# Kernel tuning notes

Hardware: AMD Instinct MI355X
Metric: run time of the kernel (lower is better)

Reference implementation:

```python
import jax, jax.numpy as jnp
import numpy as np

N, D, H, E, K = 4096, 512, 2048, 8, 2  # tokens, input/output dim, expert hidden, num_experts, top_k


def setup_inputs() -> dict:
    key = jax.random.key(0)
    k_x, k_r, k_w1, k_b1, k_w2, k_b2 = jax.random.split(key, 6)
    input_batch = jax.random.normal(k_x, (N, D), dtype=jnp.float32)
    # Router-style top-k selection: guarantees the K expert ids per token are distinct
    # (required by the torch nonzero-based dispatch) and probabilities are a softmax
    # over the selected logits, matching a standard MoE sampler.
    router_logits = jax.random.normal(k_r, (N, E), dtype=jnp.float32)
    top_vals, top_idx = jax.lax.top_k(router_logits, K)
    probabilities = jax.nn.softmax(top_vals, axis=-1)            # [N, K]
    indices = top_idx.astype(jnp.int64)                          # [N, K]
    scale = 0.02
    W1 = scale * jax.random.normal(k_w1, (E, D, H), dtype=jnp.float32)
    b1 = jnp.zeros((E, H), dtype=jnp.float32)
    W2 = scale * jax.random.normal(k_w2, (E, H, D), dtype=jnp.float32)
    b2 = jnp.zeros((E, D), dtype=jnp.float32)
    return {"input_batch": input_batch, "probabilities": probabilities, "indices": indices,
            "W1": W1, "b1": b1, "W2": W2, "b2": b2}


def reference(input_batch, probabilities, indices, W1, b1, W2, b2):
    # Each expert is a dense 2-layer GELU MLP. The torch module gathers the tokens
    # assigned to each expert, runs the expert, concatenates, sorts back to original
    # flattened [N*K] order, applies probability weighting AFTER the experts, then
    # reshapes to [N, K, D] and sums over K. That is mathematically:
    #   out[t] = sum_k probabilities[t, k] * expert_{indices[t, k]}(input_batch[t])
    h = jax.nn.gelu(jnp.einsum('nd,edh->enh', input_batch, W1) + b1[:, None, :])  # [E, N, H]
    y = jnp.einsum('enh,ehd->end', h, W2) + b2[:, None, :]                         # [E, N, D]
    y = jnp.transpose(y, (1, 0, 2))                                                # [N, E, D]
    sel = jnp.take_along_axis(y, indices[:, :, None], axis=1)                      # [N, K, D]
    output = jnp.sum(sel * probabilities[:, :, None], axis=1)                      # [N, D]
    total_loss = jnp.float32(0.0)  # no sampler / expert aux losses in this config
    return output, total_loss
```

## Files before the change

kernel.cpp:

```cpp
#include <hip/hip_runtime.h>
#include <cstdint>
#include <cstddef>

#define NTOK 4096
#define DIMD 512
#define HIDH 2048
#define NEXP 8
#define TOPK 2
#define NSLOT (NTOK*TOPK)
#define SLACK 256
#define YROWS (NSLOT+SLACK)

#define BK2 64

typedef short bf16x8_t __attribute__((ext_vector_type(8)));
typedef float f32x4_t  __attribute__((ext_vector_type(4)));

__device__ __forceinline__ unsigned short f2b(float f){
  unsigned int x = __float_as_uint(f);
  unsigned int r = (x + 0x7FFFu + ((x >> 16) & 1u)) >> 16;
  return (unsigned short)r;
}

__device__ __forceinline__ float gelu_tanh(float x) {
  float z2 = 1.5957691216057308f * fmaf(0.044715f * x, x * x, x);
  return x / (1.f + __expf(-z2));
}

__device__ __forceinline__ void gl_lds16(const void* g, void* l){
  __builtin_amdgcn_global_load_lds((const __attribute__((address_space(1))) void*)g,
                                   (__attribute__((address_space(3))) void*)l, 16, 0, 0);
}


__global__ __launch_bounds__(256) void cvt_x(const float* __restrict__ x, unsigned short* __restrict__ xb){
  int i = blockIdx.x*256 + threadIdx.x;
  if (i >= (NTOK*DIMD)/4) return;
  float4 v = ((const float4*)x)[i];
  ushort4 o; o.x=f2b(v.x); o.y=f2b(v.y); o.z=f2b(v.z); o.w=f2b(v.w);
  ((ushort4*)xb)[i] = o;
}

__global__ __launch_bounds__(256) void transpose_cvt(const float* __restrict__ src,
                                                     unsigned short* __restrict__ dst,
                                                     int R, int C){
  int e = blockIdx.z;
  src += (size_t)e*R*C; dst += (size_t)e*R*C;
  int c0 = blockIdx.x*64, r0 = blockIdx.y*64;
  __shared__ float t[64][65];
  int tr = threadIdx.x >> 4, tc = threadIdx.x & 15;
  #pragma unroll
  for (int i=0;i<4;i++){
    int r = tr + i*16;
    float4 v = *(const float4*)(src + (size_t)(r0 + r)*C + c0 + tc*4);
    t[r][tc*4+0]=v.x; t[r][tc*4+1]=v.y; t[r][tc*4+2]=v.z; t[r][tc*4+3]=v.w;
  }
  __syncthreads();
  #pragma unroll
  for (int i=0;i<4;i++){
    int c = tr + i*16;
    ushort4 o;
    o.x = f2b(t[tc*4+0][c]); o.y = f2b(t[tc*4+1][c]);
    o.z = f2b(t[tc*4+2][c]); o.w = f2b(t[tc*4+3][c]);
    *(ushort4*)(dst + (size_t)(c0 + c)*R + r0 + tc*4) = o;
  }
}


__global__ void count_k(const int* __restrict__ I, int* __restrict__ meta){
  int i = blockIdx.x*256+threadIdx.x;
  if (i < NSLOT) atomicAdd(&meta[I[i]], 1);
}
__global__ void scan_k(int* __restrict__ meta){
  if (threadIdx.x==0 && blockIdx.x==0){
    int s=0;
    for(int e=0;e<NEXP;e++){ meta[16+e]=s; s+=meta[e]; }
  }
}
__global__ void fill_k(const int* __restrict__ I, int* __restrict__ meta,
                       int* __restrict__ tokOf, int* __restrict__ rowOf){
  int i = blockIdx.x*256+threadIdx.x;
  if (i < NSLOT){
    int e = I[i];
    int pos = meta[16+e] + atomicAdd(&meta[8+e], 1);
    tokOf[pos] = i >> 1;
    rowOf[i] = pos;
  }
}



__global__ __launch_bounds__(256,2) void gemm1(
    const unsigned short* __restrict__ Xb, const unsigned short* __restrict__ W1t,
    const float* __restrict__ B1, const int* __restrict__ meta,
    const int* __restrict__ tokOf, unsigned short* __restrict__ H)
{
  const int e = blockIdx.z;
  const int cnt = meta[e];
  const int row0 = blockIdx.y * 128;
  if (row0 >= cnt) return;
  const int off = meta[16+e];
  const int h0 = blockIdx.x * 128;

  extern __shared__ unsigned short sm[];

  const int tid = threadIdx.x;
  const int tr  = tid >> 3;
  const int csw = ((tid & 7) ^ (tr & 7)) << 3;

  const unsigned short* sA[4];
  const unsigned short* sB[4];
  #pragma unroll
  for (int i=0;i<4;i++){
    int slot = min(off + row0 + i*32 + tr, NSLOT-1);
    sA[i] = Xb  + (size_t)tokOf[slot]*DIMD + csw;
    sB[i] = W1t + ((size_t)e*HIDH + h0 + i*32 + tr)*DIMD + csw;
  }

  const int lane = tid & 63, wid = tid >> 6;
  const int wr = (wid >> 1) * 64, wc = (wid & 1) * 64;
  const int l15 = lane & 15, kg = lane >> 4;
  int rowA[4], rowB[4];
  #pragma unroll
  for (int m=0;m<4;m++) rowA[m] = (wr + m*16 + l15) * BK2;
  #pragma unroll
  for (int n=0;n<4;n++) rowB[n] = (wc + n*16 + l15) * BK2;
  const int ch0 = ((kg    ) ^ (l15 & 7)) << 3;
  const int ch1 = ((kg + 4) ^ (l15 & 7)) << 3;

  f32x4_t acc[4][4];
  #pragma unroll
  for (int i=0;i<4;i++){
    #pragma unroll
    for (int j=0;j<4;j++) acc[i][j] = (f32x4_t){0.f,0.f,0.f,0.f};
  }

  auto stage = [&](int buf, int kt){
    unsigned short* d = sm + buf*16384 + tid*8;
    const int k0 = kt * BK2;
    #pragma unroll
    for (int i=0;i<4;i++){
      gl_lds16(sA[i] + k0, d + i*2048);
      gl_lds16(sB[i] + k0, d + 8192 + i*2048);
    }
  };

  auto compute = [&](int buf){
    const unsigned short* SA = sm + buf*16384;
    const unsigned short* SB = SA + 8192;
    #pragma unroll
    for (int h=0; h<2; ++h){
      const int ch = h ? ch1 : ch0;
      bf16x8_t bfr[4], af[4];
      #pragma unroll
      for (int n=0;n<4;n++) bfr[n] = *(const bf16x8_t*)&SB[rowB[n] + ch];
      #pragma unroll
      for (int m=0;m<4;m++) af[m]  = *(const bf16x8_t*)&SA[rowA[m] + ch];
      #pragma unroll
      for (int m=0;m<4;m++){
        #pragma unroll
        for (int n=0;n<4;n++)
          acc[m][n] = __builtin_amdgcn_mfma_f32_16x16x32_bf16(af[m], bfr[n], acc[m][n], 0,0,0);
      }
    }
  };

  constexpr int NS = DIMD / BK2;
  stage(0, 0);
  __syncthreads();
  for (int t = 0; t < NS; ++t){
    if (t + 1 < NS) stage((t+1) & 1, t+1);
    compute(t & 1);
    __syncthreads();
  }

  const int r4 = kg * 4;
  #pragma unroll
  for (int n=0;n<4;n++){
    const int gcol = h0 + wc + n*16 + l15;
    const float b1v = B1[(size_t)e*HIDH + gcol];
    #pragma unroll
    for (int m=0;m<4;m++){
      const int rbase = row0 + wr + m*16 + r4;
      #pragma unroll
      for (int r=0;r<4;r++){
        const int row = rbase + r;
        if (row < cnt)
          H[(size_t)(off + row)*HIDH + gcol] = f2b(gelu_tanh(acc[m][n][r] + b1v));
      }
    }
  }
}


__global__ __launch_bounds__(256,2) void gemm2(
    const unsigned short* __restrict__ Hb, const unsigned short* __restrict__ W2t,
    const int* __restrict__ meta, float* __restrict__ Y, int nsplit)
{
  const int e = blockIdx.z;
  const int cnt = meta[e];
  const int row0 = blockIdx.y * 128;
  if (row0 >= cnt) return;
  const int off = meta[16+e];
  const int ncol = DIMD / 128;
  const int d0 = (blockIdx.x % ncol) * 128;
  const int kc = blockIdx.x / ncol;
  const int kchunk = HIDH / nsplit;
  const int kbase = kc * kchunk;
  const int NS = kchunk / BK2;

  extern __shared__ unsigned short sm[];

  const int tid = threadIdx.x;
  const int tr  = tid >> 3;
  const int csw = ((tid & 7) ^ (tr & 7)) << 3;

  const unsigned short* sA[4];
  const unsigned short* sB[4];
  #pragma unroll
  for (int i=0;i<4;i++){
    int arow = min(off + row0 + i*32 + tr, YROWS-1);
    sA[i] = Hb  + (size_t)arow*HIDH + kbase + csw;
    sB[i] = W2t + ((size_t)e*DIMD + d0 + i*32 + tr)*HIDH + kbase + csw;
  }

  const int lane = tid & 63, wid = tid >> 6;
  const int wr = (wid >> 1) * 64, wc = (wid & 1) * 64;
  const int l15 = lane & 15, kg = lane >> 4;
  int rowA[4], rowB[4];
  #pragma unroll
  for (int m=0;m<4;m++) rowA[m] = (wr + m*16 + l15) * BK2;
  #pragma unroll
  for (int n=0;n<4;n++) rowB[n] = (wc + n*16 + l15) * BK2;
  const int ch0 = ((kg    ) ^ (l15 & 7)) << 3;
  const int ch1 = ((kg + 4) ^ (l15 & 7)) << 3;

  f32x4_t acc[4][4];
  #pragma unroll
  for (int i=0;i<4;i++){
    #pragma unroll
    for (int j=0;j<4;j++) acc[i][j] = (f32x4_t){0.f,0.f,0.f,0.f};
  }

  auto stage = [&](int buf, int kt){
    unsigned short* d = sm + buf*16384 + tid*8;
    const int k0 = kt * BK2;
    #pragma unroll
    for (int i=0;i<4;i++){
      gl_lds16(sA[i] + k0, d + i*2048);
      gl_lds16(sB[i] + k0, d + 8192 + i*2048);
    }
  };

  auto compute = [&](int buf){
    const unsigned short* SA = sm + buf*16384;
    const unsigned short* SB = SA + 8192;
    #pragma unroll
    for (int h=0; h<2; ++h){
      const int ch = h ? ch1 : ch0;
      bf16x8_t bfr[4], af[4];
      #pragma unroll
      for (int n=0;n<4;n++) bfr[n] = *(const bf16x8_t*)&SB[rowB[n] + ch];
      #pragma unroll
      for (int m=0;m<4;m++) af[m]  = *(const bf16x8_t*)&SA[rowA[m] + ch];
      #pragma unroll
      for (int m=0;m<4;m++){
        #pragma unroll
        for (int n=0;n<4;n++)
          acc[m][n] = __builtin_amdgcn_mfma_f32_16x16x32_bf16(af[m], bfr[n], acc[m][n], 0,0,0);
      }
    }
  };

  stage(0, 0);
  __syncthreads();
  for (int t = 0; t < NS; ++t){
    if (t + 1 < NS) stage((t+1) & 1, t+1);
    compute(t & 1);
    __syncthreads();
  }

  float* Yp = Y + (size_t)kc * YROWS * DIMD;
  const int r4 = kg * 4;
  #pragma unroll
  for (int m=0;m<4;m++){
    const int rbase = row0 + wr + m*16 + r4;
    #pragma unroll
    for (int r=0;r<4;r++){
      const int row = rbase + r;
      if (row < cnt){
        float* yp = Yp + (size_t)(off + row)*DIMD + d0 + wc + l15;
        #pragma unroll
        for (int n=0;n<4;n++) yp[n*16] = acc[m][n][r];
      }
    }
  }
}


__global__ __launch_bounds__(128) void reduce_k(
    const float* __restrict__ P, const int* __restrict__ I, const int* __restrict__ rowOf,
    const float* __restrict__ Y, const float* __restrict__ B2, float* __restrict__ out,
    int nsplit)
{
  int t = blockIdx.x; int d4 = threadIdx.x;
  float4 a = make_float4(0.f,0.f,0.f,0.f);
  #pragma unroll
  for (int k=0;k<TOPK;k++){
    int i = t*TOPK + k;
    float p = P[i]; int e = I[i]; int r = rowOf[i];
    float4 b = *(const float4*)(B2 + (size_t)e*DIMD + d4*4);
    float4 y = make_float4(b.x, b.y, b.z, b.w);
    for (int c=0;c<nsplit;c++){
      float4 v = *(const float4*)(Y + (size_t)c*YROWS*DIMD + (size_t)r*DIMD + d4*4);
      y.x += v.x; y.y += v.y; y.z += v.z; y.w += v.w;
    }
    a.x = fmaf(p, y.x, a.x); a.y = fmaf(p, y.y, a.y);
    a.z = fmaf(p, y.z, a.z); a.w = fmaf(p, y.w, a.w);
  }
  *(float4*)(out + (size_t)t*DIMD + d4*4) = a;
}


#define CAP (NTOK*TOPK)
#define ROWS 32
#define HC 64
#define NTHR 256
#define XS_LD 516
#define HS_LD 36

__global__ void fb_build(const int* __restrict__ idx, const float* __restrict__ probs,
                         int* __restrict__ counts, int* __restrict__ tok,
                         float* __restrict__ pr) {
    int i = blockIdx.x * blockDim.x + threadIdx.x;
    if (i >= NTOK * TOPK) return;
    int t = i / TOPK;
    int e = idx[i];
    float p = probs[i];
    int pos = atomicAdd(&counts[e], 1);
    tok[e * CAP + pos] = t;
    pr[e * CAP + pos] = p;
}

__global__ __launch_bounds__(NTHR)
void fb_moe(const float* __restrict__ X,
            const float* __restrict__ W1, const float* __restrict__ B1,
            const float* __restrict__ W2, const float* __restrict__ B2,
            const int* __restrict__ counts, const int* __restrict__ tok,
            const float* __restrict__ pr, float* __restrict__ out)
{
    const int e = blockIdx.y;
    const int cnt = counts[e];
    const int r0 = blockIdx.x * ROWS;
    if (r0 >= cnt) return;
    const int nr = min(ROWS, cnt - r0);

    extern __shared__ float smem[];
    float* Xs = smem;
    float* Hs = smem + ROWS * XS_LD;
    const int tid = threadIdx.x;

    for (int i = tid; i < ROWS * (DIMD / 4); i += NTHR) {
        int r = i >> 7;
        int c4 = i & 127;
        float4 v = make_float4(0.f, 0.f, 0.f, 0.f);
        if (r < nr) {
            int t = tok[e * CAP + r0 + r];
            v = *(const float4*)(X + (size_t)t * DIMD + c4 * 4);
        }
        *(float4*)(Xs + r * XS_LD + c4 * 4) = v;
    }
    __syncthreads();

    const int hq = tid & 15;
    const int rp = tid >> 4;
    const int wv = tid >> 6;
    const int ln = tid & 63;

    float yacc[8][8];
    #pragma unroll
    for (int r = 0; r < 8; ++r){
        #pragma unroll
        for (int c = 0; c < 8; ++c) yacc[r][c] = 0.f;
    }

    const float* w1base = W1 + (size_t)e * DIMD * HIDH;
    const float* w2base = W2 + (size_t)e * HIDH * DIMD;
    const float* b1base = B1 + e * HIDH;

    for (int h0 = 0; h0 < HIDH; h0 += HC) {
        float acc0[4] = {0.f, 0.f, 0.f, 0.f};
        float acc1[4] = {0.f, 0.f, 0.f, 0.f};
        const float* w1p = w1base + h0 + hq * 4;
        const float* xr0 = Xs + (rp * 2) * XS_LD;
        const float* xr1 = xr0 + XS_LD;
        #pragma unroll 2
        for (int d = 0; d < DIMD; d += 4) {
            float4 xa = *(const float4*)(xr0 + d);
            float4 xb = *(const float4*)(xr1 + d);
            float4 w0 = *(const float4*)(w1p + (size_t)(d + 0) * HIDH);
            float4 w1v = *(const float4*)(w1p + (size_t)(d + 1) * HIDH);
            float4 w2v = *(const float4*)(w1p + (size_t)(d + 2) * HIDH);
            float4 w3v = *(const float4*)(w1p + (size_t)(d + 3) * HIDH);
            float xav[4] = {xa.x, xa.y, xa.z, xa.w};
            float xbv[4] = {xb.x, xb.y, xb.z, xb.w};
            float4 wsv[4] = {w0, w1v, w2v, w3v};
            #pragma unroll
            for (int dd = 0; dd < 4; ++dd) {
                acc0[0] = fmaf(xav[dd], wsv[dd].x, acc0[0]);
                acc0[1] = fmaf(xav[dd], wsv[dd].y, acc0[1]);
                acc0[2] = fmaf(xav[dd], wsv[dd].z, acc0[2]);
                acc0[3] = fmaf(xav[dd], wsv[dd].w, acc0[3]);
                acc1[0] = fmaf(xbv[dd], wsv[dd].x, acc1[0]);
                acc1[1] = fmaf(xbv[dd], wsv[dd].y, acc1[1]);
                acc1[2] = fmaf(xbv[dd], wsv[dd].z, acc1[2]);
                acc1[3] = fmaf(xbv[dd], wsv[dd].w, acc1[3]);
            }
        }
        {
            float4 b1v = *(const float4*)(b1base + h0 + hq * 4);
            float bb[4] = {b1v.x, b1v.y, b1v.z, b1v.w};
            #pragma unroll
            for (int j = 0; j < 4; ++j) {
                Hs[(hq * 4 + j) * HS_LD + rp * 2]     = gelu_tanh(acc0[j] + bb[j]);
                Hs[(hq * 4 + j) * HS_LD + rp * 2 + 1] = gelu_tanh(acc1[j] + bb[j]);
            }
        }
        __syncthreads();

        const float* w2p = w2base + (size_t)h0 * DIMD;
        #pragma unroll 4
        for (int hc = 0; hc < HC; ++hc) {
            float4 wA = *(const float4*)(w2p + (size_t)hc * DIMD + ln * 4);
            float4 wB = *(const float4*)(w2p + (size_t)hc * DIMD + 256 + ln * 4);
            float4 hv0 = *(const float4*)(Hs + hc * HS_LD + wv * 8);
            float4 hv1 = *(const float4*)(Hs + hc * HS_LD + wv * 8 + 4);
            float hr[8] = {hv0.x, hv0.y, hv0.z, hv0.w, hv1.x, hv1.y, hv1.z, hv1.w};
            #pragma unroll
            for (int r = 0; r < 8; ++r) {
                yacc[r][0] = fmaf(hr[r], wA.x, yacc[r][0]);
                yacc[r][1] = fmaf(hr[r], wA.y, yacc[r][1]);
                yacc[r][2] = fmaf(hr[r], wA.z, yacc[r][2]);
                yacc[r][3] = fmaf(hr[r], wA.w, yacc[r][3]);
                yacc[r][4] = fmaf(hr[r], wB.x, yacc[r][4]);
                yacc[r][5] = fmaf(hr[r], wB.y, yacc[r][5]);
                yacc[r][6] = fmaf(hr[r], wB.z, yacc[r][6]);
                yacc[r][7] = fmaf(hr[r], wB.w, yacc[r][7]);
            }
        }
        __syncthreads();
    }

    const float* b2p = B2 + e * DIMD;
    float4 b2A = *(const float4*)(b2p + ln * 4);
    float4 b2B = *(const float4*)(b2p + 256 + ln * 4);
    float bA[4] = {b2A.x, b2A.y, b2A.z, b2A.w};
    float bB[4] = {b2B.x, b2B.y, b2B.z, b2B.w};
    #pragma unroll
    for (int r = 0; r < 8; ++r) {
        int rg = wv * 8 + r;
        if (rg < nr) {
            int t = tok[e * CAP + r0 + rg];
            float p = pr[e * CAP + r0 + rg];
            float* op = out + (size_t)t * DIMD;
            #pragma unroll
            for (int j = 0; j < 4; ++j) {
                atomicAdd(op + ln * 4 + j,        p * (yacc[r][j] + bA[j]));
                atomicAdd(op + 256 + ln * 4 + j,  p * (yacc[r][4 + j] + bB[j]));
            }
        }
    }
}


extern "C" void kernel_launch(void* const* d_in, const int* in_sizes, int n_in,
                              void* d_out, int out_size, void* d_ws, size_t ws_size,
                              hipStream_t stream) {
    const float* X  = (const float*)d_in[0];
    const float* P  = (const float*)d_in[1];
    const int*   I  = (const int*)d_in[2];
    const float* W1 = (const float*)d_in[3];
    const float* B1 = (const float*)d_in[4];
    const float* W2 = (const float*)d_in[5];
    const float* B2 = (const float*)d_in[6];
    float* out = (float*)d_out;
    char* ws = (char*)d_ws;

    int nsplit = 0;
    size_t o_meta=0, o_tok=0, o_row=0, o_xb=0, o_w1t=0, o_w2t=0, o_h=0, o_y=0;
    const int cand[3] = {4, 2, 1};
    for (int ci = 0; ci < 3; ++ci) {
        int ns = cand[ci];
        size_t cur = 0;
        auto alloc = [&](size_t b){ size_t p = cur; cur += (b + 255) & ~(size_t)255; return p; };
        size_t m_ = alloc(256);
        size_t t_ = alloc((size_t)NSLOT*4);
        size_t r_ = alloc((size_t)NSLOT*4);
        size_t x_ = alloc((size_t)NTOK*DIMD*2);
        size_t w1_ = alloc((size_t)NEXP*DIMD*HIDH*2);
        size_t w2_ = alloc((size_t)NEXP*DIMD*HIDH*2);
        size_t h_ = alloc((size_t)YROWS*HIDH*2);
        size_t y_ = alloc((size_t)ns*YROWS*DIMD*4);
        if (cur <= ws_size) {
            nsplit = ns;
            o_meta=m_; o_tok=t_; o_row=r_; o_xb=x_; o_w1t=w1_; o_w2t=w2_; o_h=h_; o_y=y_;
            break;
        }
    }

    if (nsplit > 0) {
        int* meta = (int*)(ws + o_meta);
        int* tokOf = (int*)(ws + o_tok);
        int* rowOf = (int*)(ws + o_row);
        unsigned short* Xb  = (unsigned short*)(ws + o_xb);
        unsigned short* W1t = (unsigned short*)(ws + o_w1t);
        unsigned short* W2t = (unsigned short*)(ws + o_w2t);
        unsigned short* Hb  = (unsigned short*)(ws + o_h);
        float* Yb = (float*)(ws + o_y);

        hipMemsetAsync(meta, 0, 256, stream);
        cvt_x<<<(NTOK*DIMD/4 + 255)/256, 256, 0, stream>>>(X, Xb);
        transpose_cvt<<<dim3(HIDH/64, DIMD/64, NEXP), 256, 0, stream>>>(W1, W1t, DIMD, HIDH);
        transpose_cvt<<<dim3(DIMD/64, HIDH/64, NEXP), 256, 0, stream>>>(W2, W2t, HIDH, DIMD);
        count_k<<<NSLOT/256, 256, 0, stream>>>(I, meta);
        scan_k<<<1, 64, 0, stream>>>(meta);
        fill_k<<<NSLOT/256, 256, 0, stream>>>(I, meta, tokOf, rowOf);

        hipFuncSetAttribute((const void*)gemm1,
                            hipFuncAttributeMaxDynamicSharedMemorySize, 65536);
        hipFuncSetAttribute((const void*)gemm2,
                            hipFuncAttributeMaxDynamicSharedMemorySize, 65536);
        gemm1<<<dim3(HIDH/128, NSLOT/128, NEXP), 256, 65536, stream>>>(
            Xb, W1t, B1, meta, tokOf, Hb);
        gemm2<<<dim3((DIMD/128)*nsplit, NSLOT/128, NEXP), 256, 65536, stream>>>(
            Hb, W2t, meta, Yb, nsplit);
        reduce_k<<<NTOK, 128, 0, stream>>>(P, I, rowOf, Yb, B2, out, nsplit);
    } else {
        int*   counts = (int*)ws;
        int*   tok    = (int*)(ws + 64);
        float* pr     = (float*)(ws + 64 + (size_t)NEXP * CAP * sizeof(int));

        hipMemsetAsync(counts, 0, NEXP * sizeof(int), stream);
        hipMemsetAsync(d_out, 0, (size_t)out_size * sizeof(float), stream);
        fb_build<<<(NTOK * TOPK + 255) / 256, 256, 0, stream>>>(I, P, counts, tok, pr);
        size_t smem = (size_t)(ROWS * XS_LD + HC * HS_LD) * sizeof(float);
        hipFuncSetAttribute((const void*)fb_moe,
                            hipFuncAttributeMaxDynamicSharedMemorySize, (int)smem);
        fb_moe<<<dim3(CAP / ROWS, NEXP), NTHR, smem, stream>>>(
            X, W1, B1, W2, B2, counts, tok, pr, out);
    }
}
```

Before: 203.5 us.

## Halve GEMM K-tile to 32, raise occupancy, and loop row blocks in fixed grid

After: 213.5 us. +4.9%, slower.

```diff
diff --git a/kernel.cpp b/kernel.cpp
--- a/kernel.cpp
+++ b/kernel.cpp
@@ -11,7 +11,7 @@
 #define SLACK 256
 #define YROWS (NSLOT+SLACK)
 
-#define BK2 64
+#define BKQ 32
 
 typedef short bf16x8_t __attribute__((ext_vector_type(8)));
 typedef float f32x4_t  __attribute__((ext_vector_type(4)));
@@ -90,208 +90,206 @@
 
 
 
-__global__ __launch_bounds__(256,2) void gemm1(
+__global__ __launch_bounds__(256,4) void gemm1(
     const unsigned short* __restrict__ Xb, const unsigned short* __restrict__ W1t,
     const float* __restrict__ B1, const int* __restrict__ meta,
     const int* __restrict__ tokOf, unsigned short* __restrict__ H)
 {
   const int e = blockIdx.z;
   const int cnt = meta[e];
-  const int row0 = blockIdx.y * 128;
-  if (row0 >= cnt) return;
   const int off = meta[16+e];
   const int h0 = blockIdx.x * 128;
 
   extern __shared__ unsigned short sm[];
 
   const int tid = threadIdx.x;
-  const int tr  = tid >> 3;
-  const int csw = ((tid & 7) ^ (tr & 7)) << 3;
-
-  const unsigned short* sA[4];
-  const unsigned short* sB[4];
-  #pragma unroll
-  for (int i=0;i<4;i++){
-    int slot = min(off + row0 + i*32 + tr, NSLOT-1);
-    sA[i] = Xb  + (size_t)tokOf[slot]*DIMD + csw;
-    sB[i] = W1t + ((size_t)e*HIDH + h0 + i*32 + tr)*DIMD + csw;
-  }
+  const int tr4 = tid >> 2;
+  const int csw = (((tid & 3) ^ ((tid >> 3) & 3)) << 3);
+
+  const unsigned short* gB0 = W1t + ((size_t)e*HIDH + h0 + tr4)*DIMD + csw;
+  const unsigned short* gB1 = gB0 + (size_t)64*DIMD;
 
   const int lane = tid & 63, wid = tid >> 6;
   const int wr = (wid >> 1) * 64, wc = (wid & 1) * 64;
   const int l15 = lane & 15, kg = lane >> 4;
-  int rowA[4], rowB[4];
-  #pragma unroll
-  for (int m=0;m<4;m++) rowA[m] = (wr + m*16 + l15) * BK2;
-  #pragma unroll
-  for (int n=0;n<4;n++) rowB[n] = (wc + n*16 + l15) * BK2;
-  const int ch0 = ((kg    ) ^ (l15 & 7)) << 3;
-  const int ch1 = ((kg + 4) ^ (l15 & 7)) << 3;
-
-  f32x4_t acc[4][4];
-  #pragma unroll
-  for (int i=0;i<4;i++){
-    #pragma unroll
-    for (int j=0;j<4;j++) acc[i][j] = (f32x4_t){0.f,0.f,0.f,0.f};
-  }
-
-  auto stage = [&](int buf, int kt){
-    unsigned short* d = sm + buf*16384 + tid*8;
-    const int k0 = kt * BK2;
+  int offA[4], offB[4];
+  #pragma unroll
+  for (int m=0;m<4;m++){
+    int r = wr + m*16 + l15;
+    offA[m] = r*BKQ + ((kg ^ ((r>>1)&3)) << 3);
+  }
+  #pragma unroll
+  for (int n=0;n<4;n++){
+    int r = wc + n*16 + l15;
+    offB[n] = r*BKQ + ((kg ^ ((r>>1)&3)) << 3);
+  }
+
+  for (int rb = blockIdx.y; rb * 128 < cnt; rb += gridDim.y) {
+    const int row0 = rb * 128;
+    const int s0 = min(off + row0 + tr4,      NSLOT-1);
+    const int s1 = min(off + row0 + 64 + tr4, NSLOT-1);
+    const unsigned short* gA0 = Xb + (size_t)tokOf[s0]*DIMD + csw;
+    const unsigned short* gA1 = Xb + (size_t)tokOf[s1]*DIMD + csw;
+
+    f32x4_t acc[4][4];
     #pragma unroll
     for (int i=0;i<4;i++){
-      gl_lds16(sA[i] + k0, d + i*2048);
-      gl_lds16(sB[i] + k0, d + 8192 + i*2048);
-    }
-  };
-
-  auto compute = [&](int buf){
-    const unsigned short* SA = sm + buf*16384;
-    const unsigned short* SB = SA + 8192;
-    #pragma unroll
-    for (int h=0; h<2; ++h){
-      const int ch = h ? ch1 : ch0;
-      bf16x8_t bfr[4], af[4];
-      #pragma unroll
-      for (int n=0;n<4;n++) bfr[n] = *(const bf16x8_t*)&SB[rowB[n] + ch];
-      #pragma unroll
-      for (int m=0;m<4;m++) af[m]  = *(const bf16x8_t*)&SA[rowA[m] + ch];
+      #pragma unroll
+      for (int j=0;j<4;j++) acc[i][j] = (f32x4_t){0.f,0.f,0.f,0.f};
+    }
+
+    auto stage = [&](int buf, int kt){
+      unsigned short* d = sm + buf*8192 + tid*8;
+      const int k0 = kt * BKQ;
+      gl_lds16(gA0 + k0, d);
+      gl_lds16(gA1 + k0, d + 2048);
+      gl_lds16(gB0 + k0, d + 4096);
+      gl_lds16(gB1 + k0, d + 4096 + 2048);
+    };
+
+    auto compute = [&](int buf){
+      const unsigned short* SA = sm + buf*8192;
+      const unsigned short* SB = SA + 4096;
+      bf16x8_t af[4], bfr[4];
+      #pragma unroll
+      for (int n=0;n<4;n++) bfr[n] = *(const bf16x8_t*)&SB[offB[n]];
+      #pragma unroll
+      for (int m=0;m<4;m++) af[m]  = *(const bf16x8_t*)&SA[offA[m]];
       #pragma unroll
       for (int m=0;m<4;m++){
         #pragma unroll
         for (int n=0;n<4;n++)
           acc[m][n] = __builtin_amdgcn_mfma_f32_16x16x32_bf16(af[m], bfr[n], acc[m][n], 0,0,0);
       }
-    }
-  };
-
-  constexpr int NS = DIMD / BK2;
-  stage(0, 0);
-  __syncthreads();
-  for (int t = 0; t < NS; ++t){
-    if (t + 1 < NS) stage((t+1) & 1, t+1);
-    compute(t & 1);
+    };
+
+    constexpr int NS = DIMD / BKQ;
+    stage(0, 0);
     __syncthreads();
-  }
-
-  const int r4 = kg * 4;
-  #pragma unroll
-  for (int n=0;n<4;n++){
-    const int gcol = h0 + wc + n*16 + l15;
-    const float b1v = B1[(size_t)e*HIDH + gcol];
+    for (int t = 0; t < NS; ++t){
+      if (t + 1 < NS) stage((t+1) & 1, t+1);
+      compute(t & 1);
+      __syncthreads();
+    }
+
+    const int r4 = kg * 4;
     #pragma unroll
-    for (int m=0;m<4;m++){
-      const int rbase = row0 + wr + m*16 + r4;
-      #pragma unroll
-      for (int r=0;r<4;r++){
-        const int row = rbase + r;
-        if (row < cnt)
-          H[(size_t)(off + row)*HIDH + gcol] = f2b(gelu_tanh(acc[m][n][r] + b1v));
+    for (int n=0;n<4;n++){
+      const int gcol = h0 + wc + n*16 + l15;
+      const float b1v = B1[(size_t)e*HIDH + gcol];
+      #pragma unroll
+      for (int m=0;m<4;m++){
+        const int rbase = row0 + wr + m*16 + r4;
+        #pragma unroll
+        for (int r=0;r<4;r++){
+          const int row = rbase + r;
+          if (row < cnt)
+            H[(size_t)(off + row)*HIDH + gcol] = f2b(gelu_tanh(acc[m][n][r] + b1v));
+        }
       }
     }
   }
 }
 
 
-__global__ __launch_bounds__(256,2) void gemm2(
+__global__ __launch_bounds__(256,4) void gemm2(
     const unsigned short* __restrict__ Hb, const unsigned short* __restrict__ W2t,
     const int* __restrict__ meta, float* __restrict__ Y, int nsplit)
 {
   const int e = blockIdx.z;
   const int cnt = meta[e];
-  const int row0 = blockIdx.y * 128;
-  if (row0 >= cnt) return;
   const int off = meta[16+e];
   const int ncol = DIMD / 128;
   const int d0 = (blockIdx.x % ncol) * 128;
   const int kc = blockIdx.x / ncol;
   const int kchunk = HIDH / nsplit;
   const int kbase = kc * kchunk;
-  const int NS = kchunk / BK2;
+  const int NS = kchunk / BKQ;
 
   extern __shared__ unsigned short sm[];
 
   const int tid = threadIdx.x;
-  const int tr  = tid >> 3;
-  const int csw = ((tid & 7) ^ (tr & 7)) << 3;
-
-  const unsigned short* sA[4];
-  const unsigned short* sB[4];
-  #pragma unroll
-  for (int i=0;i<4;i++){
-    int arow = min(off + row0 + i*32 + tr, YROWS-1);
-    sA[i] = Hb  + (size_t)arow*HIDH + kbase + csw;
-    sB[i] = W2t + ((size_t)e*DIMD + d0 + i*32 + tr)*HIDH + kbase + csw;
-  }
+  const int tr4 = tid >> 2;
+  const int csw = (((tid & 3) ^ ((tid >> 3) & 3)) << 3);
+
+  const unsigned short* gB0 = W2t + ((size_t)e*DIMD + d0 + tr4)*HIDH + kbase + csw;
+  const unsigned short* gB1 = gB0 + (size_t)64*HIDH;
 
   const int lane = tid & 63, wid = tid >> 6;
   const int wr = (wid >> 1) * 64, wc = (wid & 1) * 64;
   const int l15 = lane & 15, kg = lane >> 4;
-  int rowA[4], rowB[4];
-  #pragma unroll
-  for (int m=0;m<4;m++) rowA[m] = (wr + m*16 + l15) * BK2;
-  #pragma unroll
-  for (int n=0;n<4;n++) rowB[n] = (wc + n*16 + l15) * BK2;
-  const int ch0 = ((kg    ) ^ (l15 & 7)) << 3;
-  const int ch1 = ((kg + 4) ^ (l15 & 7)) << 3;
-
-  f32x4_t acc[4][4];
-  #pragma unroll
-  for (int i=0;i<4;i++){
-    #pragma unroll
-    for (int j=0;j<4;j++) acc[i][j] = (f32x4_t){0.f,0.f,0.f,0.f};
-  }
-
-  auto stage = [&](int buf, int kt){
-    unsigned short* d = sm + buf*16384 + tid*8;
-    const int k0 = kt * BK2;
+  int offA[4], offB[4];
+  #pragma unroll
+  for (int m=0;m<4;m++){
+    int r = wr + m*16 + l15;
+    offA[m] = r*BKQ + ((kg ^ ((r>>1)&3)) << 3);
+  }
+  #pragma unroll
+  for (int n=0;n<4;n++){
+    int r = wc + n*16 + l15;
+    offB[n] = r*BKQ + ((kg ^ ((r>>1)&3)) << 3);
+  }
+
+  for (int rb = blockIdx.y; rb * 128 < cnt; rb += gridDim.y) {
+    const int row0 = rb * 128;
+    const int a0 = min(off + row0 + tr4,      YROWS-1);
+    const int a1 = min(off + row0 + 64 + tr4, YROWS-1);
+    const unsigned short* gA0 = Hb + (size_t)a0*HIDH + kbase + csw;
+    const unsigned short* gA1 = Hb + (size_t)a1*HIDH + kbase + csw;
+
+    f32x4_t acc[4][4];
     #pragma unroll
     for (int i=0;i<4;i++){
-      gl_lds16(sA[i] + k0, d + i*2048);
-      gl_lds16(sB[i] + k0, d + 8192 + i*2048);
-    }
-  };
-
-  auto compute = [&](int buf){
-    const unsigned short* SA = sm + buf*16384;
-    const unsigned short* SB = SA + 8192;
-    #pragma unroll
-    for (int h=0; h<2; ++h){
-      const int ch = h ? ch1 : ch0;
-      bf16x8_t bfr[4], af[4];
-      #pragma unroll
-      for (int n=0;n<4;n++) bfr[n] = *(const bf16x8_t*)&SB[rowB[n] + ch];
-      #pragma unroll
-      for (int m=0;m<4;m++) af[m]  = *(const bf16x8_t*)&SA[rowA[m] + ch];
+      #pragma unroll
+      for (int j=0;j<4;j++) acc[i][j] = (f32x4_t){0.f,0.f,0.f,0.f};
+    }
+
+    auto stage = [&](int buf, int kt){
+      unsigned short* d = sm + buf*8192 + tid*8;
+      const int k0 = kt * BKQ;
+      gl_lds16(gA0 + k0, d);
+      gl_lds16(gA1 + k0, d + 2048);
+      gl_lds16(gB0 + k0, d + 4096);
+      gl_lds16(gB1 + k0, d + 4096 + 2048);
+    };
+
+    auto compute = [&](int buf){
+      const unsigned short* SA = sm + buf*8192;
+      const unsigned short* SB = SA + 4096;
+      bf16x8_t af[4], bfr[4];
+      #pragma unroll
+      for (int n=0;n<4;n++) bfr[n] = *(const bf16x8_t*)&SB[offB[n]];
+      #pragma unroll
+      for (int m=0;m<4;m++) af[m]  = *(const bf16x8_t*)&SA[offA[m]];
       #pragma unroll
       for (int m=0;m<4;m++){
         #pragma unroll
         for (int n=0;n<4;n++)
           acc[m][n] = __builtin_amdgcn_mfma_f32_16x16x32_bf16(af[m], bfr[n], acc[m][n], 0,0,0);
       }
-    }
-  };
-
-  stage(0, 0);
-  __syncthreads();
-  for (int t = 0; t < NS; ++t){
-    if (t + 1 < NS) stage((t+1) & 1, t+1);
-    compute(t & 1);
+    };
+
+    stage(0, 0);
     __syncthreads();
-  }
-
-  float* Yp = Y + (size_t)kc * YROWS * DIMD;
-  const int r4 = kg * 4;
-  #pragma unroll
-  for (int m=0;m<4;m++){
-    const int rbase = row0 + wr + m*16 + r4;
+    for (int t = 0; t < NS; ++t){
+      if (t + 1 < NS) stage((t+1) & 1, t+1);
+      compute(t & 1);
+      __syncthreads();
+    }
+
+    float* Yp = Y + (size_t)kc * YROWS * DIMD;
+    const int r4 = kg * 4;
     #pragma unroll
-    for (int r=0;r<4;r++){
-      const int row = rbase + r;
-      if (row < cnt){
-        float* yp = Yp + (size_t)(off + row)*DIMD + d0 + wc + l15;
-        #pragma unroll
-        for (int n=0;n<4;n++) yp[n*16] = acc[m][n][r];
+    for (int m=0;m<4;m++){
+      const int rbase = row0 + wr + m*16 + r4;
+      #pragma unroll
+      for (int r=0;r<4;r++){
+        const int row = rbase + r;
+        if (row < cnt){
+          float* yp = Yp + (size_t)(off + row)*DIMD + d0 + wc + l15;
+          #pragma unroll
+          for (int n=0;n<4;n++) yp[n*16] = acc[m][n][r];
+        }
       }
     }
   }
@@ -527,12 +525,12 @@
         fill_k<<<NSLOT/256, 256, 0, stream>>>(I, meta, tokOf, rowOf);
 
         hipFuncSetAttribute((const void*)gemm1,
-                            hipFuncAttributeMaxDynamicSharedMemorySize, 65536);
+                            hipFuncAttributeMaxDynamicSharedMemorySize, 32768);
         hipFuncSetAttribute((const void*)gemm2,
-                            hipFuncAttributeMaxDynamicSharedMemorySize, 65536);
-        gemm1<<<dim3(HIDH/128, NSLOT/128, NEXP), 256, 65536, stream>>>(
+                            hipFuncAttributeMaxDynamicSharedMemorySize, 32768);
+        gemm1<<<dim3(HIDH/128, 16, NEXP), 256, 32768, stream>>>(
             Xb, W1t, B1, meta, tokOf, Hb);
-        gemm2<<<dim3((DIMD/128)*nsplit, NSLOT/128, NEXP), 256, 65536, stream>>>(
+        gemm2<<<dim3((DIMD/128)*nsplit, 16, NEXP), 256, 32768, stream>>>(
             Hb, W2t, meta, Yb, nsplit);
         reduce_k<<<NTOK, 128, 0, stream>>>(P, I, rowOf, Yb, B2, out, nsplit);
     } else {
```
